# Kernel optimization log

Measured on AMD Instinct MI355X. Metric: run time of the kernel, lower is better.

Reference implementation:

```python
import jax, jax.numpy as jnp
import numpy as np

DIM = 1024
HEADS = 16
HEAD_DIM = DIM // HEADS
SCALE = HEAD_DIM ** -0.5


def setup_inputs() -> dict:
    key = jax.random.key(0)
    k_x, k_wqkv, k_bqkv, k_wp, k_bp = jax.random.split(key, 5)
    B, N, C = 8, 1024, DIM
    lim_qkv = 1.0 / np.sqrt(C)
    x = jax.random.normal(k_x, (B, N, C), dtype=jnp.float32)
    # store weights in [in, out] layout (torch Linear weight is [out,in]; y = x @ W.T + b)
    W_qkv = jax.random.uniform(k_wqkv, (C, 3 * C), dtype=jnp.float32, minval=-lim_qkv, maxval=lim_qkv)
    b_qkv = jax.random.uniform(k_bqkv, (3 * C,), dtype=jnp.float32, minval=-lim_qkv, maxval=lim_qkv)
    W_proj = jax.random.uniform(k_wp, (C, C), dtype=jnp.float32, minval=-lim_qkv, maxval=lim_qkv)
    b_proj = jax.random.uniform(k_bp, (C,), dtype=jnp.float32, minval=-lim_qkv, maxval=lim_qkv)
    return {"x": x, "W_qkv": W_qkv, "b_qkv": b_qkv, "W_proj": W_proj, "b_proj": b_proj}


def reference(x, W_qkv, b_qkv, W_proj, b_proj):
    B, N, C = x.shape
    H, D = HEADS, C // HEADS
    qkv = x @ W_qkv + b_qkv                          # [B, N, 3C]
    qkv = qkv.reshape(B, N, 3, H, D)
    q, k, v = jnp.moveaxis(qkv, 2, 0)                # each [B, N, H, D]
    q = q.transpose(0, 2, 1, 3)                      # [B, H, N, D]
    k = k.transpose(0, 2, 1, 3)
    v = v.transpose(0, 2, 1, 3)
    attn = jnp.einsum("bhnd,bhmd->bhnm", q, k) * SCALE
    attn = jax.nn.softmax(attn, axis=-1)
    out = jnp.einsum("bhnm,bhmd->bhnd", attn, v)     # [B, H, N, D]
    out = out.transpose(0, 2, 1, 3).reshape(B, N, C)
    return out @ W_proj + b_proj
```

## Files before the change

### kernel.cpp

```cpp
#include <hip/hip_runtime.h>
#include <hip/hip_bf16.h>


using bf16x8 = __attribute__((ext_vector_type(8))) short;
using f32x4  = __attribute__((ext_vector_type(4))) float;
using u16    = unsigned short;
using u16x8  = __attribute__((ext_vector_type(8))) unsigned short;
using u32x2  = __attribute__((ext_vector_type(2))) unsigned int;

__device__ __forceinline__ u16 f2bf(float f) {
  unsigned int u = __float_as_uint(f);
  u += 0x7FFFu + ((u >> 16) & 1u);
  return (u16)(u >> 16);
}
__device__ __forceinline__ float bf2f(u16 h) {
  return __uint_as_float(((unsigned int)h) << 16);
}
__device__ __forceinline__ unsigned cvt_pk_bf16(float a, float b) {
  unsigned r;
  asm("v_cvt_pk_bf16_f32 %0, %1, %2" : "=v"(r) : "v"(a), "v"(b));
  return r;
}
__device__ __forceinline__ float fexp2(float x) {
#if __has_builtin(__builtin_amdgcn_exp2f)
  return __builtin_amdgcn_exp2f(x);
#else
  return exp2f(x);
#endif
}

__device__ __forceinline__ void gload16(const u16* g, u16* lbase, int lane) {
#if __has_builtin(__builtin_amdgcn_global_load_lds)
  __builtin_amdgcn_global_load_lds(
      (const __attribute__((address_space(1))) void*)g,
      (__attribute__((address_space(3))) void*)lbase, 16, 0, 0);
#else
  *(u16x8*)(lbase + (size_t)lane * 8) = *(const u16x8*)g;
#endif
}

__device__ __forceinline__ void transpose_tile(
    const float* __restrict__ W, u16* __restrict__ Wt, int K, int N,
    int n0, int k0, float (*T)[65], int t)
{
  const int r = t >> 4, c4 = (t & 15) * 4;
  #pragma unroll
  for (int i = 0; i < 4; ++i) {
    f32x4 v = *(const f32x4*)&W[(size_t)(k0 + r + i * 16) * N + n0 + c4];
    T[r + i * 16][c4 + 0] = v.x;
    T[r + i * 16][c4 + 1] = v.y;
    T[r + i * 16][c4 + 2] = v.z;
    T[r + i * 16][c4 + 3] = v.w;
  }
  __syncthreads();
  const int nr = t >> 2, cs = (t & 3) * 16;
  u16x8 h0, h1;
  #pragma unroll
  for (int j = 0; j < 8; ++j) h0[j] = f2bf(T[cs + j][nr]);
  #pragma unroll
  for (int j = 0; j < 8; ++j) h1[j] = f2bf(T[cs + 8 + j][nr]);
  u16* dst = Wt + (size_t)(n0 + nr) * K + k0 + cs;
  *(u16x8*)dst = h0;
  *(u16x8*)(dst + 8) = h1;
}

__global__ __launch_bounds__(256) void prep(
    const float* __restrict__ x, u16* __restrict__ Xb,
    const float* __restrict__ Wq, u16* __restrict__ Wqt,
    const float* __restrict__ Wp, u16* __restrict__ Wpt)
{
  __shared__ float T[64][65];
  const int bid = blockIdx.x, t = threadIdx.x;
  if (bid < 4096) {
    size_t i = ((size_t)bid * 256 + t) * 8;
    f32x4 a = *(const f32x4*)(x + i);
    f32x4 b = *(const f32x4*)(x + i + 4);
    u16x8 h = { f2bf(a.x), f2bf(a.y), f2bf(a.z), f2bf(a.w),
                f2bf(b.x), f2bf(b.y), f2bf(b.z), f2bf(b.w) };
    *(u16x8*)(Xb + i) = h;
  } else if (bid < 4864) {
    const int tb = bid - 4096;
    transpose_tile(Wq, Wqt, 1024, 3072, (tb % 48) * 64, (tb / 48) * 64, T, t);
  } else {
    const int tb = bid - 4864;
    transpose_tile(Wp, Wpt, 1024, 1024, (tb % 16) * 64, (tb / 16) * 64, T, t);
  }
}

#define GEMM64_LOOP(ABASE, BBASE, AS, BS)                                     \
  const int tid = threadIdx.x;                                                \
  const int lane = tid & 63, wid = tid >> 6;                                  \
  const int wr = wid >> 1, wc = wid & 1;                                      \
  const int lg = lane >> 4, lc = lane & 15;                                   \
  const int row0 = blockIdx.x * 128, col0 = blockIdx.y * 128;                 \
  f32x4 acc[4][4];                                                            \
  _Pragma("unroll")                                                           \
  for (int m = 0; m < 4; ++m)                                                 \
    _Pragma("unroll")                                                         \
    for (int n = 0; n < 4; ++n) acc[m][n] = (f32x4){0.f, 0.f, 0.f, 0.f};      \
  const int srow = lane >> 3;                                       \
  const int sslot = (lane & 7) ^ srow;             \
  const u16* gA = (ABASE) + (size_t)(row0 + wid * 32 + srow) * 1024 + sslot * 8; \
  const u16* gB = (BBASE) + (size_t)(col0 + wid * 32 + srow) * 1024 + sslot * 8; \
  u16* lA = (AS) + wid * 2048;                                                \
  u16* lB = (BS) + wid * 2048;                                                \
  const int xr = lc & 7;                                                      \
  const int sl0 = ((0 + lg) ^ xr) * 8, sl1 = ((4 + lg) ^ xr) * 8;             \
  const int arow = (wr * 64 + lc) * 64, brow = (wc * 64 + lc) * 64;           \
  for (int k0 = 0; k0 < 1024; k0 += 64) {                                     \
    _Pragma("unroll")                                                         \
    for (int c = 0; c < 4; ++c) {                                             \
      gload16(gA + (size_t)c * 8192 + k0, lA + c * 512, lane);                \
      gload16(gB + (size_t)c * 8192 + k0, lB + c * 512, lane);                \
    }                                                                         \
    __syncthreads();                                                          \
    _Pragma("unroll")                                                         \
    for (int ks = 0; ks < 2; ++ks) {                                          \
      const int sl = ks ? sl1 : sl0;                                          \
      bf16x8 a[4], b[4];                                                      \
      _Pragma("unroll")                                                       \
      for (int m = 0; m < 4; ++m)                                             \
        a[m] = *(const bf16x8*)((AS) + arow + m * 1024 + sl);                 \
      _Pragma("unroll")                                                       \
      for (int n = 0; n < 4; ++n)                                             \
        b[n] = *(const bf16x8*)((BS) + brow + n * 1024 + sl);                 \
      __builtin_amdgcn_s_setprio(1);                                          \
      _Pragma("unroll")                                                       \
      for (int m = 0; m < 4; ++m)                                             \
        _Pragma("unroll")                                                     \
        for (int n = 0; n < 4; ++n)                                           \
          acc[m][n] = __builtin_amdgcn_mfma_f32_16x16x32_bf16(                \
              a[m], b[n], acc[m][n], 0, 0, 0);                                \
      __builtin_amdgcn_s_setprio(0);                                          \
    }                                                                         \
    __syncthreads();                                                          \
  }

__global__ __launch_bounds__(256, 2) void qkv_gemm2(
    const u16* __restrict__ Xb, const u16* __restrict__ Wt,
    const float* __restrict__ bias,
    u16* __restrict__ Qb, u16* __restrict__ Kb, u16* __restrict__ VtG)
{
  __shared__ __align__(16) u16 SM[128 * 130];
  u16* As = SM;
  u16* Bs = SM + 8192;
  u16* Tv = SM;

  GEMM64_LOOP(Xb, Wt, As, Bs)

  const int which = col0 >> 10;
  if (which == 2) {
    #pragma unroll
    for (int m = 0; m < 4; ++m) {
      #pragma unroll
      for (int n = 0; n < 4; ++n) {
        const int col = wc * 64 + n * 16 + lc;
        const float bv = bias[col0 + col];
        const int rrow = wr * 64 + m * 16 + lg * 4;
        #pragma unroll
        for (int r = 0; r < 4; ++r)
          Tv[(rrow + r) * 130 + col] = f2bf(acc[m][n][r] + bv);
      }
    }
    __syncthreads();
    const int c = tid >> 1, half = tid & 1;
    const int hh = c >> 6, d = c & 63;
    const int bb = row0 >> 10, nb = row0 & 1023;
    const int hbase = (col0 & 1023) >> 6;
    u16* vdst = VtG + ((size_t)(bb * 16 + hbase + hh) * 64 + d) * 1024
                + nb + half * 64;
    #pragma unroll
    for (int g = 0; g < 8; ++g) {
      u16x8 o;
      #pragma unroll
      for (int j = 0; j < 8; ++j)
        o[j] = Tv[(half * 64 + g * 8 + j) * 130 + c];
      *(u16x8*)(vdst + g * 8) = o;
    }
  } else {
    u16* dst = (which == 0) ? Qb : Kb;
    #pragma unroll
    for (int m = 0; m < 4; ++m) {
      #pragma unroll
      for (int n = 0; n < 4; ++n) {
        const int gc = col0 + wc * 64 + n * 16 + lc;
        const float bv = bias[gc];
        const int ci = gc & 1023, h = ci >> 6, d = ci & 63;
        const int gr0 = row0 + wr * 64 + m * 16 + lg * 4;
        const int bb = gr0 >> 10, nn0 = gr0 & 1023;
        #pragma unroll
        for (int r = 0; r < 4; ++r)
          dst[((size_t)(bb * 16 + h) * 1024 + nn0 + r) * 64 + d] =
              f2bf(acc[m][n][r] + bv);
      }
    }
  }
}

__global__ __launch_bounds__(512, 1) void attn_kernel(
    const u16* __restrict__ Q, const u16* __restrict__ K,
    const u16* __restrict__ Vt, u16* __restrict__ O)
{
  __shared__ __align__(16) u16 Ks[64 * 64];
  __shared__ __align__(16) u16 Vs[64 * 64];
  __shared__ __align__(16) u16 Pl[8 * 32 * 72];

  const int tid = threadIdx.x, lane = tid & 63, wid = tid >> 6;
  const int lg = lane >> 4, lc = lane & 15;
  const int bh = blockIdx.x;
  const int qt = blockIdx.y;
  const size_t base = (size_t)bh * 65536;
  const u16* Qp = Q + base;
  const u16* Kp = K + base;
  const u16* Vp = Vt + base;

  const float QSCALE = 0.125f * 1.44269504f;
  bf16x8 qf[2][2];
  #pragma unroll
  for (int f = 0; f < 2; ++f) {
    const u16* qsrc = Qp + (size_t)(qt * 256 + wid * 32 + f * 16 + lc) * 64 + lg * 8;
    #pragma unroll
    for (int ks = 0; ks < 2; ++ks) {
      u16x8 raw = *(const u16x8*)(qsrc + ks * 32);
      bf16x8 t;
      #pragma unroll
      for (int j = 0; j < 8; ++j) t[j] = (short)f2bf(bf2f(raw[j]) * QSCALE);
      qf[f][ks] = t;
    }
  }

  f32x4 o[2][4];
  #pragma unroll
  for (int f = 0; f < 2; ++f)
    #pragma unroll
    for (int d = 0; d < 4; ++d) o[f][d] = (f32x4){0.f, 0.f, 0.f, 0.f};
  float m_r[2] = {-1e30f, -1e30f};
  float l_r[2] = {0.f, 0.f};

  const int srow  = lane >> 3;
  const int sslot = (lane & 7) ^ srow;
  const u16* gK0 = Kp + (size_t)(wid * 8 + srow) * 64 + sslot * 8;
  const u16* gV0 = Vp + (size_t)(wid * 8 + srow) * 1024 + sslot * 8;
  u16* lK0 = Ks + wid * 512;
  u16* lV0 = Vs + wid * 512;

  const int xr = lc & 7;
  const int cof0 = ((0 + lg) ^ xr) * 8;
  const int cof1 = ((4 + lg) ^ xr) * 8;
  const int prow = (wid * 32 + lc) * 72;

  for (int kt = 0; kt < 16; ++kt) {
    gload16(gK0 + kt * 4096, lK0, lane);
    gload16(gV0 + kt * 64, lV0, lane);
    __syncthreads();

    f32x4 s[2][4];
    #pragma unroll
    for (int f = 0; f < 2; ++f)
      #pragma unroll
      for (int kb = 0; kb < 4; ++kb) s[f][kb] = (f32x4){0.f, 0.f, 0.f, 0.f};
    #pragma unroll
    for (int ks = 0; ks < 2; ++ks) {
      const int co = ks ? cof1 : cof0;
      #pragma unroll
      for (int kb = 0; kb < 4; ++kb) {
        bf16x8 kfr = *(const bf16x8*)(Ks + (kb * 16 + lc) * 64 + co);
        s[0][kb] = __builtin_amdgcn_mfma_f32_16x16x32_bf16(kfr, qf[0][ks], s[0][kb], 0, 0, 0);
        s[1][kb] = __builtin_amdgcn_mfma_f32_16x16x32_bf16(kfr, qf[1][ks], s[1][kb], 0, 0, 0);
      }
    }

    #pragma unroll
    for (int f = 0; f < 2; ++f) {
      f32x4 t01, t23;
      #pragma unroll
      for (int c = 0; c < 4; ++c) {
        t01[c] = fmaxf(s[f][0][c], s[f][1][c]);
        t23[c] = fmaxf(s[f][2][c], s[f][3][c]);
      }
      float t = fmaxf(fmaxf(fmaxf(t01[0], t01[1]), fmaxf(t01[2], t01[3])),
                      fmaxf(fmaxf(t23[0], t23[1]), fmaxf(t23[2], t23[3])));
      t = fmaxf(t, __shfl_xor(t, 16));
      t = fmaxf(t, __shfl_xor(t, 32));

      if (!__all((t - m_r[f]) <= 11.5f)) {
        float nm = fmaxf(m_r[f], t);
        float sc = fexp2(m_r[f] - nm);
        m_r[f] = nm;
        l_r[f] *= sc;
        #pragma unroll
        for (int r = 0; r < 4; ++r) {
          float scr = __shfl(sc, lg * 4 + r, 16);
          #pragma unroll
          for (int d = 0; d < 4; ++d) o[f][d][r] *= scr;
        }
      }

      float lsum = 0.f;
      #pragma unroll
      for (int kb = 0; kb < 4; ++kb) {
        f32x4 p;
        #pragma unroll
        for (int c = 0; c < 4; ++c) {
          p[c] = fexp2(s[f][kb][c] - m_r[f]);
          lsum += p[c];
        }
        u32x2 w = { cvt_pk_bf16(p[0], p[1]), cvt_pk_bf16(p[2], p[3]) };
        *(u32x2*)(Pl + prow + f * 1152 + kb * 16 + lg * 4) = w;
      }
      l_r[f] += lsum;
    }

    asm volatile("s_waitcnt lgkmcnt(0)" ::: "memory");
    __builtin_amdgcn_sched_barrier(0);

    bf16x8 pa[2][2];
    #pragma unroll
    for (int f = 0; f < 2; ++f)
      #pragma unroll
      for (int ks = 0; ks < 2; ++ks)
        pa[f][ks] = *(const bf16x8*)(Pl + prow + f * 1152 + ks * 32 + lg * 8);
    #pragma unroll
    for (int d = 0; d < 4; ++d) {
      #pragma unroll
      for (int ks = 0; ks < 2; ++ks) {
        const int co = ks ? cof1 : cof0;
        bf16x8 vfr = *(const bf16x8*)(Vs + (d * 16 + lc) * 64 + co);
        o[0][d] = __builtin_amdgcn_mfma_f32_16x16x32_bf16(pa[0][ks], vfr, o[0][d], 0, 0, 0);
        o[1][d] = __builtin_amdgcn_mfma_f32_16x16x32_bf16(pa[1][ks], vfr, o[1][d], 0, 0, 0);
      }
    }
    __syncthreads();
  }

  const int b = bh >> 4, h = bh & 15;
  #pragma unroll
  for (int f = 0; f < 2; ++f) {
    float t = l_r[f];
    t += __shfl_xor(t, 16);
    t += __shfl_xor(t, 32);
    float linv = 1.0f / t;
    #pragma unroll
    for (int r = 0; r < 4; ++r) {
      float li = __shfl(linv, lg * 4 + r, 16);
      int n = qt * 256 + wid * 32 + f * 16 + lg * 4 + r;
      u16* dst = O + ((size_t)b * 1024 + n) * 1024 + h * 64 + lc;
      #pragma unroll
      for (int d = 0; d < 4; ++d) dst[d * 16] = f2bf(o[f][d][r] * li);
    }
  }
}

__global__ __launch_bounds__(256, 2) void proj_gemm2(
    const u16* __restrict__ Ab, const u16* __restrict__ Wt,
    const float* __restrict__ bias, float* __restrict__ Out)
{
  __shared__ __align__(16) u16 As[128 * 64];
  __shared__ __align__(16) u16 Bs[128 * 64];

  GEMM64_LOOP(Ab, Wt, As, Bs)

  #pragma unroll
  for (int m = 0; m < 4; ++m) {
    #pragma unroll
    for (int n = 0; n < 4; ++n) {
      #pragma unroll
      for (int r = 0; r < 4; ++r) {
        int gr = row0 + wr * 64 + m * 16 + lg * 4 + r;
        int gc = col0 + wc * 64 + n * 16 + lc;
        Out[(size_t)gr * 1024 + gc] = acc[m][n][r] + bias[gc];
      }
    }
  }
}

extern "C" void kernel_launch(void* const* d_in, const int* in_sizes, int n_in,
                              void* d_out, int out_size, void* d_ws, size_t ws_size,
                              hipStream_t stream) {
  const float* x     = (const float*)d_in[0];
  const float* W_qkv = (const float*)d_in[1];
  const float* b_qkv = (const float*)d_in[2];
  const float* W_prj = (const float*)d_in[3];
  const float* b_prj = (const float*)d_in[4];
  float* out = (float*)d_out;

  const size_t SEG = (size_t)8192 * 1024;
  char* ws = (char*)d_ws;
  u16* Xb  = (u16*)ws;
  u16* Ab  = Xb;
  u16* VtG = (u16*)(ws + SEG * 2);
  u16* Wqt = (u16*)(ws + SEG * 4);
  u16* Wpt = Wqt + (size_t)3072 * 1024;
  u16* Qb  = (u16*)d_out;
  u16* Kb  = Qb + SEG;

  prep<<<5120, 256, 0, stream>>>(x, Xb, W_qkv, Wqt, W_prj, Wpt);
  qkv_gemm2<<<dim3(64, 24), 256, 0, stream>>>(Xb, Wqt, b_qkv, Qb, Kb, VtG);
  attn_kernel<<<dim3(128, 4), 512, 0, stream>>>(Qb, Kb, VtG, Ab);
  proj_gemm2<<<dim3(64, 8), 256, 0, stream>>>(Ab, Wpt, b_prj, out);
}
```

Measured before the change: 149.2 us.

## Double-buffer LDS tiles in QKV and proj GEMMs to overlap loads with MFMA

The shared GEMM main loop now uses two LDS buffers per operand. The next K-tile is issued with global-to-LDS loads before the current tile is computed, and partial vmcnt waits plus raw s_barrier replace the full __syncthreads pair. The goal is to hide global load latency behind MFMA work. In exchange, LDS use per block doubles to 64 KB, which may limit the two-blocks-per-CU occupancy target.

```diff
diff --git a/kernel.cpp b/kernel.cpp
--- a/kernel.cpp
+++ b/kernel.cpp
@@ -87,7 +87,7 @@
   }
 }
 
-#define GEMM64_LOOP(ABASE, BBASE, AS, BS)                                     \
+#define GEMM64_DBUF(ABASE, BBASE, AS, BS)                                     \
   const int tid = threadIdx.x;                                                \
   const int lane = tid & 63, wid = tid >> 6;                                  \
   const int wr = wid >> 1, wc = wid & 1;                                      \
@@ -104,26 +104,37 @@
   const u16* gB = (BBASE) + (size_t)(col0 + wid * 32 + srow) * 1024 + sslot * 8; \
   u16* lA = (AS) + wid * 2048;                                                \
   u16* lB = (BS) + wid * 2048;                                                \
+  auto STAGE = [&](int tt) {                                                  \
+    const int bo = (tt & 1) * 8192, ko = tt * 64;                             \
+    _Pragma("unroll")                                                         \
+    for (int c = 0; c < 4; ++c) {                                             \
+      gload16(gA + (size_t)c * 8192 + ko, lA + bo + c * 512, lane);           \
+      gload16(gB + (size_t)c * 8192 + ko, lB + bo + c * 512, lane);           \
+    }                                                                         \
+  };                                                                          \
+  STAGE(0);                                                                   \
   const int xr = lc & 7;                                                      \
   const int sl0 = ((0 + lg) ^ xr) * 8, sl1 = ((4 + lg) ^ xr) * 8;             \
   const int arow = (wr * 64 + lc) * 64, brow = (wc * 64 + lc) * 64;           \
-  for (int k0 = 0; k0 < 1024; k0 += 64) {                                     \
-    _Pragma("unroll")                                                         \
-    for (int c = 0; c < 4; ++c) {                                             \
-      gload16(gA + (size_t)c * 8192 + k0, lA + c * 512, lane);                \
-      gload16(gB + (size_t)c * 8192 + k0, lB + c * 512, lane);                \
+  for (int t = 0; t < 16; ++t) {                                              \
+    if (t < 15) {                                                             \
+      STAGE(t + 1);                                                           \
+      asm volatile("s_waitcnt vmcnt(8)" ::: "memory");                        \
+    } else {                                                                  \
+      asm volatile("s_waitcnt vmcnt(0)" ::: "memory");                        \
     }                                                                         \
-    __syncthreads();                                                          \
+    __builtin_amdgcn_s_barrier();                                             \
+    const int bo = (t & 1) * 8192;                                            \
     _Pragma("unroll")                                                         \
     for (int ks = 0; ks < 2; ++ks) {                                          \
       const int sl = ks ? sl1 : sl0;                                          \
       bf16x8 a[4], b[4];                                                      \
       _Pragma("unroll")                                                       \
       for (int m = 0; m < 4; ++m)                                             \
-        a[m] = *(const bf16x8*)((AS) + arow + m * 1024 + sl);                 \
+        a[m] = *(const bf16x8*)((AS) + bo + arow + m * 1024 + sl);            \
       _Pragma("unroll")                                                       \
       for (int n = 0; n < 4; ++n)                                             \
-        b[n] = *(const bf16x8*)((BS) + brow + n * 1024 + sl);                 \
+        b[n] = *(const bf16x8*)((BS) + bo + brow + n * 1024 + sl);            \
       __builtin_amdgcn_s_setprio(1);                                          \
       _Pragma("unroll")                                                       \
       for (int m = 0; m < 4; ++m)                                             \
@@ -133,7 +144,7 @@
               a[m], b[n], acc[m][n], 0, 0, 0);                                \
       __builtin_amdgcn_s_setprio(0);                                          \
     }                                                                         \
-    __syncthreads();                                                          \
+    __builtin_amdgcn_s_barrier();                                             \
   }
 
 __global__ __launch_bounds__(256, 2) void qkv_gemm2(
@@ -141,12 +152,12 @@
     const float* __restrict__ bias,
     u16* __restrict__ Qb, u16* __restrict__ Kb, u16* __restrict__ VtG)
 {
-  __shared__ __align__(16) u16 SM[128 * 130];
+  __shared__ __align__(16) u16 SM[32768];
   u16* As = SM;
-  u16* Bs = SM + 8192;
+  u16* Bs = SM + 16384;
   u16* Tv = SM;
 
-  GEMM64_LOOP(Xb, Wt, As, Bs)
+  GEMM64_DBUF(Xb, Wt, As, Bs)
 
   const int which = col0 >> 10;
   if (which == 2) {
@@ -355,10 +366,10 @@
     const u16* __restrict__ Ab, const u16* __restrict__ Wt,
     const float* __restrict__ bias, float* __restrict__ Out)
 {
-  __shared__ __align__(16) u16 As[128 * 64];
-  __shared__ __align__(16) u16 Bs[128 * 64];
-
-  GEMM64_LOOP(Ab, Wt, As, Bs)
+  __shared__ __align__(16) u16 As[2 * 128 * 64];
+  __shared__ __align__(16) u16 Bs[2 * 128 * 64];
+
+  GEMM64_DBUF(Ab, Wt, As, Bs)
 
   #pragma unroll
   for (int m = 0; m < 4; ++m) {
```

After: 145.3 us, median of 2. 1.03x faster.
